# Kernel optimization log

Measured on AMD Instinct MI355X. Metric: run time of the kernel, lower is better.

## Reference

```python
import jax, jax.numpy as jnp
import numpy as np
import math

EPS = 1e-8        # numeric guard in segment intersection (matches mmcv EPSILON)
MODE_EPS = 1e-6   # module's eps
N_BOXES = 1000000


def box2corners(box):
    # box: (B, N, 5) -> corners (B, N, 4, 2)
    cx, cy, w, h, a = [box[..., i:i + 1] for i in range(5)]
    x4 = jnp.asarray([0.5, -0.5, -0.5, 0.5], box.dtype) * w   # (B,N,4)
    y4 = jnp.asarray([-0.5, -0.5, 0.5, 0.5], box.dtype) * h
    c, s = jnp.cos(a), jnp.sin(a)
    return jnp.stack([x4 * c - y4 * s + cx, x4 * s + y4 * c + cy], axis=-1)


def box_intersection(corners1, corners2):
    # all pairwise segment intersections between edges of the two boxes
    line1 = jnp.concatenate([corners1, jnp.roll(corners1, -1, axis=2)], axis=-1)  # (B,N,4,4)
    line2 = jnp.concatenate([corners2, jnp.roll(corners2, -1, axis=2)], axis=-1)
    l1 = line1[:, :, :, None, :]  # (B,N,4,1,4)
    l2 = line2[:, :, None, :, :]  # (B,N,1,4,4)
    x1, y1, x2, y2 = l1[..., 0], l1[..., 1], l1[..., 2], l1[..., 3]
    x3, y3, x4, y4 = l2[..., 0], l2[..., 1], l2[..., 2], l2[..., 3]
    num = (y4 - y3) * (x2 - x1) - (x4 - x3) * (y2 - y1)
    den_t = (x4 - x3) * (y1 - y3) - (y4 - y3) * (x1 - x3)
    t = den_t / (num + EPS)
    t_chk = jnp.where(num == 0, -1.0, t)
    mask_t = (t_chk > 0) & (t_chk < 1)
    den_u = (x2 - x1) * (y1 - y3) - (y2 - y1) * (x1 - x3)
    u = -den_u / (num + EPS)
    u_chk = jnp.where(num == 0, -1.0, u)
    mask_u = (u_chk > 0) & (u_chk < 1)
    mask = mask_t & mask_u  # (B,N,4,4)
    pts = jnp.stack([x1 + t * (x2 - x1), y1 + t * (y2 - y1)], axis=-1)
    pts = pts * mask[..., None].astype(pts.dtype)
    return pts, mask  # (B,N,4,4,2), (B,N,4,4)


def box_in_box(corners1, corners2):
    # which corners of box1 lie inside box2 (projection test)
    a = corners2[:, :, 0:1, :]
    b = corners2[:, :, 1:2, :]
    d = corners2[:, :, 3:4, :]
    ab, ad, am = b - a, d - a, corners1 - a
    p_ab = jnp.sum(ab * am, -1) / jnp.sum(ab * ab, -1)
    p_ad = jnp.sum(ad * am, -1) / jnp.sum(ad * ad, -1)
    tol = 1e-6
    return (p_ab > -tol) & (p_ab < 1 + tol) & (p_ad > -tol) & (p_ad < 1 + tol)


def intersection_area(corners1, corners2):
    # differentiable convex-intersection area via vertex sort + shoelace
    inter_pts, inter_mask = box_intersection(corners1, corners2)
    c1_in_2 = box_in_box(corners1, corners2)
    c2_in_1 = box_in_box(corners2, corners1)
    B, N = corners1.shape[:2]
    verts = jnp.concatenate([corners1, corners2, inter_pts.reshape(B, N, 16, 2)], axis=2)  # (B,N,24,2)
    mask = jnp.concatenate([c1_in_2, c2_in_1, inter_mask.reshape(B, N, 16)], axis=2)       # (B,N,24)
    num_valid = jnp.sum(mask, axis=-1, keepdims=True).astype(verts.dtype)  # (B,N,1)
    center = jnp.sum(verts * mask[..., None], axis=2) / jnp.maximum(num_valid, 1.0)  # (B,N,2)
    v = verts - center[:, :, None, :]
    ang = jnp.where(mask, jnp.arctan2(v[..., 1], v[..., 0]), 1e7)  # invalid -> end
    order = jnp.argsort(ang, axis=-1)
    v_sorted = jnp.take_along_axis(v, order[..., None], axis=2)
    m_sorted = jnp.take_along_axis(mask, order, axis=2)
    first = v_sorted[:, :, 0:1, :]
    poly = jnp.where(m_sorted[..., None], v_sorted, first)  # pad with first vertex (closes polygon)
    nxt = jnp.roll(poly, -1, axis=2)
    cross = poly[..., 0] * nxt[..., 1] - poly[..., 1] * nxt[..., 0]
    return jnp.abs(jnp.sum(cross, axis=-1)) * 0.5  # (B,N)


def diff_iou_rotated_2d(box1, box2):
    c1, c2 = box2corners(box1), box2corners(box2)
    inter = intersection_area(c1, c2)
    area1 = box1[..., 2] * box1[..., 3]
    area2 = box2[..., 2] * box2[..., 3]
    return inter / (area1 + area2 - inter)


def obb2hbb_xyxy(obb):
    cx, cy, w, h, a = obb[:, 0], obb[:, 1], obb[:, 2], obb[:, 3], obb[:, 4]
    c, s = jnp.abs(jnp.cos(a)), jnp.abs(jnp.sin(a))
    dw = (w * c + h * s) * 0.5
    dh = (w * s + h * c) * 0.5
    return jnp.stack([cx - dw, cy - dh, cx + dw, cy + dh], axis=-1)


def setup_inputs():
    key = jax.random.key(0)
    k = jax.random.split(key, 7)
    N = N_BOXES
    cxy = jax.random.uniform(k[0], (N, 2), jnp.float32, 0.0, 1024.0)
    wh = jax.random.uniform(k[1], (N, 2), jnp.float32, 8.0, 128.0)
    ang = jax.random.uniform(k[2], (N, 1), jnp.float32, -np.pi / 2, np.pi / 2)
    pred = jnp.concatenate([cxy, wh, ang], axis=-1)
    jit_xy = jax.random.uniform(k[3], (N, 2), jnp.float32, -10.0, 10.0)
    jit_wh = jax.random.uniform(k[4], (N, 2), jnp.float32, 0.8, 1.25)
    jit_a = jax.random.uniform(k[5], (N, 1), jnp.float32, -0.3, 0.3)
    target = jnp.concatenate([pred[:, :2] + jit_xy, pred[:, 2:4] * jit_wh, pred[:, 4:5] + jit_a], axis=-1)
    weight = jax.random.uniform(k[6], (N,), jnp.float32, 0.5, 1.5)
    return {"pred": pred, "target": target, "weight": weight}


def reference(pred, target, weight):
    eps = MODE_EPS
    ious = jnp.clip(diff_iou_rotated_2d(pred[None], target[None])[0], 0.0, 1.0)  # (N,)
    # enclosing HBB for penalty terms
    hp, ht = obb2hbb_xyxy(pred), obb2hbb_xyxy(target)
    en_wh = jnp.clip(jnp.maximum(hp[:, 2:], ht[:, 2:]) - jnp.minimum(hp[:, :2], ht[:, :2]), 0.0)
    c2 = en_wh[:, 0] ** 2 + en_wh[:, 1] ** 2 + eps
    rho2 = (target[:, 0] - pred[:, 0]) ** 2 + (target[:, 1] - pred[:, 1]) ** 2
    factor = 4.0 / (math.pi ** 2)
    v = factor * (jnp.arctan(target[:, 2] / (target[:, 3] + eps)) - jnp.arctan(pred[:, 2] / (pred[:, 3] + eps))) ** 2
    alpha = jax.lax.stop_gradient((ious > 0.5).astype(v.dtype) * v / (1.0 - ious + v + eps))
    cious = ious - (jnp.clip(rho2 / c2, 0.0, 1.0) + alpha * v)
    loss = (1.0 - cious) * weight
    return jnp.mean(loss)  # loss_weight=1.0, reduction='mean'
```

## Files before the change

kernel.cpp:

```cpp
#include <hip/hip_runtime.h>
#include <math.h>


#define BLOCK 256
#define NV 16
#define LDS_STRIDE 17

typedef float v2f __attribute__((ext_vector_type(2)));

struct CEList {
    int n;
    unsigned char lo[128];
    unsigned char hi[128];
};

constexpr CEList make_ces16() {
    CEList L{};
    L.n = 0;
    for (int p = 1; p < NV; p <<= 1)
        for (int k = p; k >= 1; k >>= 1)
            for (int j = k % p; j + k < NV; j += 2 * k)
                for (int i = 0; i < k; i++) {
                    int lo = i + j, hi = i + j + k;
                    if (hi < NV && (lo / (2 * p)) == (hi / (2 * p))) {
                        L.lo[L.n] = (unsigned char)lo;
                        L.hi[L.n] = (unsigned char)hi;
                        L.n++;
                    }
                }
    return L;
}

constexpr CEList CES = make_ces16();

__device__ __forceinline__ float frcp(float x) {
    return __builtin_amdgcn_rcpf(x);
}

__device__ __forceinline__ v2f splat2(float x) {
    v2f r; r.x = x; r.y = x; return r;
}

__device__ __forceinline__ float hadd2(v2f v) { return v.x + v.y; }

__device__ __forceinline__ float angle_key(float x, float y) {
    float ax = fabsf(x), ay = fabsf(y);
    float den = ax + ay;
    float r = x * frcp(den);
    r = (den > 0.f) ? r : 0.f;
    return (y >= 0.f) ? (1.f - r) : (3.f + r);
}

__device__ __forceinline__ unsigned int pack_bf2(float x, float y) {
    unsigned int bx = __float_as_uint(x) + 0x8000u;
    unsigned int by = __float_as_uint(y) + 0x8000u;
    return (by & 0xFFFF0000u) | (bx >> 16);
}

__device__ __forceinline__ float atan01(float z) {
    float z2 = z * z;
    float p = -0.01172120f;
    p = p * z2 + 0.05265332f;
    p = p * z2 - 0.11643287f;
    p = p * z2 + 0.19354346f;
    p = p * z2 - 0.33262347f;
    p = p * z2 + 0.99997726f;
    return z * p;
}

__device__ __forceinline__ float pair_loss(const float* __restrict__ p,
                                           const float* __restrict__ t,
                                           float wv,
                                           unsigned int* __restrict__ myb)
{
    const float EPSf  = 1e-8f;
    const float TOLf  = 1e-6f;
    const float MEPS  = 1e-6f;
    const float PIf   = 3.14159265358979323846f;

    float pcx = p[0], pcy = p[1], pw = p[2], ph = p[3], pa = p[4];
    float tcx = t[0], tcy = t[1], tw = t[2], th = t[3], ta = t[4];

    float ca = __cosf(pa), sa = __sinf(pa);
    float cb = __cosf(ta), sb = __sinf(ta);
    v2f C1[4], C2[4];
    {
        const float xs[4] = { 0.5f, -0.5f, -0.5f, 0.5f };
        const float ys[4] = { -0.5f, -0.5f, 0.5f, 0.5f };
        v2f R1x = { ca, sa },  R1y = { -sa, cb };
        R1y.x = -sa; R1y.y = ca;
        v2f R2x = { cb, sb },  R2y = { -sb, cb };
        R2y.x = -sb; R2y.y = cb;
        v2f CT1 = { pcx, pcy }, CT2 = { tcx, tcy };
        #pragma unroll
        for (int k = 0; k < 4; k++) {
            float x4 = xs[k] * pw, y4 = ys[k] * ph;
            C1[k] = splat2(x4) * R1x + splat2(y4) * R1y + CT1;
            float x4b = xs[k] * tw, y4b = ys[k] * th;
            C2[k] = splat2(x4b) * R2x + splat2(y4b) * R2y + CT2;
        }
    }

    v2f  V[NV];
    bool msk[NV];

    {
        v2f A  = C2[0];
        v2f AB = C2[1] - A, AD = C2[3] - A;
        float rab = frcp(hadd2(AB * AB));
        float rad = frcp(hadd2(AD * AD));
        #pragma unroll
        for (int k = 0; k < 4; k++) {
            v2f AM = C1[k] - A;
            float pab = hadd2(AB * AM) * rab;
            float pad = hadd2(AD * AM) * rad;
            msk[k] = (pab > -TOLf) && (pab < 1.f + TOLf) &&
                     (pad > -TOLf) && (pad < 1.f + TOLf);
            V[k] = C1[k];
        }
    }
    {
        v2f A  = C1[0];
        v2f AB = C1[1] - A, AD = C1[3] - A;
        float rab = frcp(hadd2(AB * AB));
        float rad = frcp(hadd2(AD * AD));
        #pragma unroll
        for (int k = 0; k < 4; k++) {
            v2f AM = C2[k] - A;
            float pab = hadd2(AB * AM) * rab;
            float pad = hadd2(AD * AM) * rad;
            msk[4 + k] = (pab > -TOLf) && (pab < 1.f + TOLf) &&
                         (pad > -TOLf) && (pad < 1.f + TOLf);
            V[4 + k] = C2[k];
        }
    }
    #pragma unroll
    for (int e1 = 0; e1 < 4; e1++) {
        v2f P1 = C1[e1];
        v2f E  = C1[(e1 + 1) & 3] - P1;
        v2f  Q[4];
        bool qm[4];
        #pragma unroll
        for (int e2 = 0; e2 < 4; e2++) {
            v2f P3 = C2[e2];
            v2f F  = C2[(e2 + 1) & 3] - P3;
            float num  = F.y * E.x - F.x * E.y;
            float rnum = frcp(num + EPSf);
            v2f D = P1 - P3;
            float den_t = F.x * D.y - F.y * D.x;
            float den_u = E.x * D.y - E.y * D.x;
            float tt = den_t * rnum;
            float uu = -den_u * rnum;
            qm[e2] = (num != 0.f) && (tt > 0.f) && (tt < 1.f)
                                  && (uu > 0.f) && (uu < 1.f);
            Q[e2] = splat2(tt) * E + P1;
        }
        bool mfL = qm[0] || qm[1];
        v2f  fL  = qm[0] ? Q[0] : Q[1];
        bool msL = qm[0] && qm[1];
        bool mfR = qm[2] || qm[3];
        v2f  fR  = qm[2] ? Q[2] : Q[3];
        bool msR = qm[2] && qm[3];
        int s0 = 8 + 2 * e1, s1 = s0 + 1;
        V[s0]   = mfL ? fL : fR;
        msk[s0] = mfL || mfR;
        v2f  t2 = msL ? Q[1] : fR;
        V[s1]   = mfL ? t2 : Q[3];
        msk[s1] = msL || (mfL && mfR) || msR;
    }

    v2f s2 = { 0.f, 0.f };
    float cnt = 0.f;
    const v2f Z2 = { 0.f, 0.f };
    #pragma unroll
    for (int k = 0; k < NV; k++) {
        s2  += msk[k] ? V[k] : Z2;
        cnt += msk[k] ? 1.f : 0.f;
    }
    float rden = frcp(fmaxf(cnt, 1.f));
    v2f cen = s2 * splat2(rden);

    unsigned int ku[NV];
    #pragma unroll
    for (int k = 0; k < NV; k++) {
        v2f R = V[k] - cen;
        myb[k] = pack_bf2(R.x, R.y);
        float a = msk[k] ? angle_key(R.x, R.y) : 1e7f;
        ku[k] = (__float_as_uint(a) & 0xFFFFFFF0u) | (unsigned int)k;
    }

    #pragma unroll
    for (int c = 0; c < CES.n; c++) {
        const int lo = CES.lo[c], hi = CES.hi[c];
        unsigned int a = ku[lo], b = ku[hi];
        ku[lo] = a < b ? a : b;
        ku[hi] = a < b ? b : a;
    }

    const unsigned int VALID_LIM = 0x49742400u;
    float gx[NV], gy[NV];
    bool  gv[NV];
    #pragma unroll
    for (int k = 0; k < NV; k++) {
        unsigned int pk = myb[ku[k] & 15u];
        gx[k] = __uint_as_float(pk << 16);
        gy[k] = __uint_as_float(pk & 0xFFFF0000u);
        gv[k] = ku[k] < VALID_LIM;
    }
    float fx = gx[0], fy = gy[0];
    float cross = 0.f;
    #pragma unroll
    for (int k = 0; k < NV; k++) {
        int kn = (k + 1) % NV;
        float axv = gv[k]  ? gx[k]  : fx, ayv = gv[k]  ? gy[k]  : fy;
        float bxv = gv[kn] ? gx[kn] : fx, byv = gv[kn] ? gy[kn] : fy;
        cross += axv * byv - ayv * bxv;
    }
    float inter = fabsf(cross) * 0.5f;

    float area1 = pw * ph, area2 = tw * th;
    float iou = inter * frcp(area1 + area2 - inter);
    iou = fminf(fmaxf(iou, 0.f), 1.f);

    float cA = fabsf(ca), sA = fabsf(sa);
    float cB = fabsf(cb), sB = fabsf(sb);
    float dw1 = (pw * cA + ph * sA) * 0.5f, dh1 = (pw * sA + ph * cA) * 0.5f;
    float dw2 = (tw * cB + th * sB) * 0.5f, dh2 = (tw * sB + th * cB) * 0.5f;
    float hp0 = pcx - dw1, hp1 = pcy - dh1, hp2 = pcx + dw1, hp3 = pcy + dh1;
    float ht0 = tcx - dw2, ht1 = tcy - dh2, ht2 = tcx + dw2, ht3 = tcy + dh2;

    float enw = fmaxf(fmaxf(hp2, ht2) - fminf(hp0, ht0), 0.f);
    float enh = fmaxf(fmaxf(hp3, ht3) - fminf(hp1, ht1), 0.f);
    float c2v = enw * enw + enh * enh + MEPS;
    float rho2 = (tcx - pcx) * (tcx - pcx) + (tcy - pcy) * (tcy - pcy);

    float factor = 4.f / (PIf * PIf);
    float r1 = tw * frcp(th + MEPS);
    float r2 = pw * frcp(ph + MEPS);
    float xd = (r1 - r2) * frcp(1.f + r1 * r2);
    float axd = fabsf(xd);
    bool  big = axd > 1.f;
    float z   = big ? frcp(axd) : axd;
    float at  = atan01(z);
    float dv  = big ? ((0.5f * PIf) - at) : at;
    float v_ = factor * dv * dv;
    float alpha = (iou > 0.5f) ? v_ * frcp(1.f - iou + v_ + MEPS) : 0.f;

    float rhoterm = fminf(fmaxf(rho2 * frcp(c2v), 0.f), 1.f);
    float ciou = iou - (rhoterm + alpha * v_);
    return (1.f - ciou) * wv;
}

__global__ __launch_bounds__(BLOCK)
void obb_ciou_kernel(const float* __restrict__ pred,
                     const float* __restrict__ tgt,
                     const float* __restrict__ wgt,
                     float* __restrict__ out,
                     int N, float invN)
{
    __shared__ unsigned int slab[BLOCK * LDS_STRIDE];
    unsigned int* myb = slab + (int)threadIdx.x * LDS_STRIDE;

    int i = blockIdx.x * BLOCK + (int)threadIdx.x;
    float loss = 0.f;
    if (i < N)
        loss = pair_loss(pred + (size_t)i * 5, tgt + (size_t)i * 5,
                         wgt[i], myb);

    #pragma unroll
    for (int off = 32; off > 0; off >>= 1)
        loss += __shfl_down(loss, off, 64);

    __shared__ float red[BLOCK / 64];
    int wave = threadIdx.x >> 6;
    int lane = threadIdx.x & 63;
    if (lane == 0) red[wave] = loss;
    __syncthreads();
    if (threadIdx.x == 0) {
        float s = 0.f;
        #pragma unroll
        for (int w = 0; w < BLOCK / 64; w++) s += red[w];
        atomicAdd(out, s * invN);
    }
}

extern "C" void kernel_launch(void* const* d_in, const int* in_sizes, int n_in,
                              void* d_out, int out_size, void* d_ws, size_t ws_size,
                              hipStream_t stream) {
    const float* pred = (const float*)d_in[0];
    const float* tgt  = (const float*)d_in[1];
    const float* wgt  = (const float*)d_in[2];
    float* out = (float*)d_out;
    int N = in_sizes[2];

    hipMemsetAsync(out, 0, sizeof(float) * (size_t)out_size, stream);

    int grid = (N + BLOCK - 1) / BLOCK;
    obb_ciou_kernel<<<grid, BLOCK, 0, stream>>>(pred, tgt, wgt, out, N,
                                                1.f / (float)N);
}
```

Measured before the change: 133.1 us.

## Compute box intersection in pred-box local frame to simplify geometry

Transforms the target box into the predicted box's local coordinate frame, so the predicted box becomes axis-aligned. Corner-in-box tests turn into absolute-value comparisons, and edge intersections reduce to one-dimensional solves against constant lines with precomputed reciprocals. This cuts the per-pair ALU and reciprocal work of the general segment-intersection code. The tolerance semantics change slightly (scaled half-extent bounds instead of projection tolerances, and no epsilon guard on the denominator), which could alter masks for degenerate or edge-touching cases.

```diff
diff --git a/kernel.cpp b/kernel.cpp
--- a/kernel.cpp
+++ b/kernel.cpp
@@ -37,12 +37,6 @@
     return __builtin_amdgcn_rcpf(x);
 }
 
-__device__ __forceinline__ v2f splat2(float x) {
-    v2f r; r.x = x; r.y = x; return r;
-}
-
-__device__ __forceinline__ float hadd2(v2f v) { return v.x + v.y; }
-
 __device__ __forceinline__ float angle_key(float x, float y) {
     float ax = fabsf(x), ay = fabsf(y);
     float den = ax + ay;
@@ -73,100 +67,108 @@
                                            float wv,
                                            unsigned int* __restrict__ myb)
 {
-    const float EPSf  = 1e-8f;
-    const float TOLf  = 1e-6f;
-    const float MEPS  = 1e-6f;
-    const float PIf   = 3.14159265358979323846f;
+    const float MEPS = 1e-6f;
+    const float PIf  = 3.14159265358979323846f;
+    const float TOLm = 1.f + 2e-6f;
 
     float pcx = p[0], pcy = p[1], pw = p[2], ph = p[3], pa = p[4];
     float tcx = t[0], tcy = t[1], tw = t[2], th = t[3], ta = t[4];
 
     float ca = __cosf(pa), sa = __sinf(pa);
     float cb = __cosf(ta), sb = __sinf(ta);
-    v2f C1[4], C2[4];
-    {
-        const float xs[4] = { 0.5f, -0.5f, -0.5f, 0.5f };
-        const float ys[4] = { -0.5f, -0.5f, 0.5f, 0.5f };
-        v2f R1x = { ca, sa },  R1y = { -sa, cb };
-        R1y.x = -sa; R1y.y = ca;
-        v2f R2x = { cb, sb },  R2y = { -sb, cb };
-        R2y.x = -sb; R2y.y = cb;
-        v2f CT1 = { pcx, pcy }, CT2 = { tcx, tcy };
-        #pragma unroll
-        for (int k = 0; k < 4; k++) {
-            float x4 = xs[k] * pw, y4 = ys[k] * ph;
-            C1[k] = splat2(x4) * R1x + splat2(y4) * R1y + CT1;
-            float x4b = xs[k] * tw, y4b = ys[k] * th;
-            C2[k] = splat2(x4b) * R2x + splat2(y4b) * R2y + CT2;
-        }
-    }
+
+    float hw1 = 0.5f * pw, hh1 = 0.5f * ph;
+    float hw2 = 0.5f * tw, hh2 = 0.5f * th;
+
+    float ddx = tcx - pcx, ddy = tcy - pcy;
+    float c2x = ddx * ca + ddy * sa;
+    float c2y = ddy * ca - ddx * sa;
+    float cd  = cb * ca + sb * sa;
+    float sd  = sb * ca - cb * sa;
+
+    float Axv = hw2 * cd,  Ayv = hw2 * sd;
+    float Bxv = -hh2 * sd, Byv = hh2 * cd;
+    float qpAx = c2x + Axv, qpAy = c2y + Ayv;
+    float qmAx = c2x - Axv, qmAy = c2y - Ayv;
+    float C0x = qpAx - Bxv, C0y = qpAy - Byv;
+    float C1x = qmAx - Bxv, C1y = qmAy - Byv;
+    float C2x = qmAx + Bxv, C2y = qmAy + Byv;
+    float C3x = qpAx + Bxv, C3y = qpAy + Byv;
 
     v2f  V[NV];
     bool msk[NV];
 
     {
-        v2f A  = C2[0];
-        v2f AB = C2[1] - A, AD = C2[3] - A;
-        float rab = frcp(hadd2(AB * AB));
-        float rad = frcp(hadd2(AD * AD));
+        float exl = -hw1 - c2x, exh = hw1 - c2x;
+        float eyl = -hh1 - c2y, eyh = hh1 - c2y;
+        float lw2 = hw2 * TOLm, lh2 = hh2 * TOLm;
+        float du, dv;
+        du = exh * cd + eyl * sd; dv = eyl * cd - exh * sd;
+        msk[0] = (fabsf(du) < lw2) && (fabsf(dv) < lh2);
+        V[0] = (v2f){ hw1, -hh1 };
+        du = exl * cd + eyl * sd; dv = eyl * cd - exl * sd;
+        msk[1] = (fabsf(du) < lw2) && (fabsf(dv) < lh2);
+        V[1] = (v2f){ -hw1, -hh1 };
+        du = exl * cd + eyh * sd; dv = eyh * cd - exl * sd;
+        msk[2] = (fabsf(du) < lw2) && (fabsf(dv) < lh2);
+        V[2] = (v2f){ -hw1, hh1 };
+        du = exh * cd + eyh * sd; dv = eyh * cd - exh * sd;
+        msk[3] = (fabsf(du) < lw2) && (fabsf(dv) < lh2);
+        V[3] = (v2f){ hw1, hh1 };
+    }
+
+    {
+        float lw1 = hw1 * TOLm, lh1 = hh1 * TOLm;
+        msk[4] = (fabsf(C0x) < lw1) && (fabsf(C0y) < lh1); V[4] = (v2f){C0x, C0y};
+        msk[5] = (fabsf(C1x) < lw1) && (fabsf(C1y) < lh1); V[5] = (v2f){C1x, C1y};
+        msk[6] = (fabsf(C2x) < lw1) && (fabsf(C2y) < lh1); V[6] = (v2f){C2x, C2y};
+        msk[7] = (fabsf(C3x) < lw1) && (fabsf(C3y) < lh1); V[7] = (v2f){C3x, C3y};
+    }
+
+    {
+        float twcd = Axv + Axv, twsd = Ayv + Ayv;
+        float thsd = -(Bxv + Bxv), thcd = Byv + Byv;
+        float rax = frcp(twcd), ray = frcp(twsd);
+        float rbx = frcp(thsd), rby = frcp(thcd);
+
+        float Sx[4]  = { C0x, C1x, C2x, C3x };
+        float Sy[4]  = { C0y, C1y, C2y, C3y };
+        float Dxe[4] = { -twcd, -thsd, twcd, thsd };
+        float Dye[4] = { -twsd, thcd, twsd, -thcd };
+        float iDx[4] = { -rax, -rbx, rax, rbx };
+        float iDy[4] = { -ray, rby, ray, -rby };
+
         #pragma unroll
-        for (int k = 0; k < 4; k++) {
-            v2f AM = C1[k] - A;
-            float pab = hadd2(AB * AM) * rab;
-            float pad = hadd2(AD * AM) * rad;
-            msk[k] = (pab > -TOLf) && (pab < 1.f + TOLf) &&
-                     (pad > -TOLf) && (pad < 1.f + TOLf);
-            V[k] = C1[k];
+        for (int e1 = 0; e1 < 4; e1++) {
+            const bool horiz = (e1 == 0) || (e1 == 2);
+            const float cc   = (e1 == 0) ? -hh1 : (e1 == 1) ? -hw1
+                             : (e1 == 2) ?  hh1 :  hw1;
+            const float lim  = horiz ? hw1 : hh1;
+            float q[4]; bool qm[4];
+            #pragma unroll
+            for (int j = 0; j < 4; j++) {
+                float u = horiz ? (cc - Sy[j]) * iDy[j]
+                                : (cc - Sx[j]) * iDx[j];
+                float w = horiz ? fmaf(u, Dxe[j], Sx[j])
+                                : fmaf(u, Dye[j], Sy[j]);
+                qm[j] = (u > -1.f) && (u < 0.f) && (fabsf(w) < lim);
+                q[j] = w;
+            }
+            bool mfL = qm[0] || qm[1];
+            float fL = qm[0] ? q[0] : q[1];
+            bool msL = qm[0] && qm[1];
+            bool mfR = qm[2] || qm[3];
+            float fR = qm[2] ? q[2] : q[3];
+            bool msR = qm[2] && qm[3];
+            int s0 = 8 + 2 * e1, s1 = s0 + 1;
+            float w0 = mfL ? fL : fR;
+            msk[s0]  = mfL || mfR;
+            float t2v = msL ? q[1] : fR;
+            float w1 = mfL ? t2v : q[3];
+            msk[s1]  = msL || (mfL && mfR) || msR;
+            V[s0] = horiz ? (v2f){ w0, cc } : (v2f){ cc, w0 };
+            V[s1] = horiz ? (v2f){ w1, cc } : (v2f){ cc, w1 };
         }
-    }
-    {
-        v2f A  = C1[0];
-        v2f AB = C1[1] - A, AD = C1[3] - A;
-        float rab = frcp(hadd2(AB * AB));
-        float rad = frcp(hadd2(AD * AD));
-        #pragma unroll
-        for (int k = 0; k < 4; k++) {
-            v2f AM = C2[k] - A;
-            float pab = hadd2(AB * AM) * rab;
-            float pad = hadd2(AD * AM) * rad;
-            msk[4 + k] = (pab > -TOLf) && (pab < 1.f + TOLf) &&
-                         (pad > -TOLf) && (pad < 1.f + TOLf);
-            V[4 + k] = C2[k];
-        }
-    }
-    #pragma unroll
-    for (int e1 = 0; e1 < 4; e1++) {
-        v2f P1 = C1[e1];
-        v2f E  = C1[(e1 + 1) & 3] - P1;
-        v2f  Q[4];
-        bool qm[4];
-        #pragma unroll
-        for (int e2 = 0; e2 < 4; e2++) {
-            v2f P3 = C2[e2];
-            v2f F  = C2[(e2 + 1) & 3] - P3;
-            float num  = F.y * E.x - F.x * E.y;
-            float rnum = frcp(num + EPSf);
-            v2f D = P1 - P3;
-            float den_t = F.x * D.y - F.y * D.x;
-            float den_u = E.x * D.y - E.y * D.x;
-            float tt = den_t * rnum;
-            float uu = -den_u * rnum;
-            qm[e2] = (num != 0.f) && (tt > 0.f) && (tt < 1.f)
-                                  && (uu > 0.f) && (uu < 1.f);
-            Q[e2] = splat2(tt) * E + P1;
-        }
-        bool mfL = qm[0] || qm[1];
-        v2f  fL  = qm[0] ? Q[0] : Q[1];
-        bool msL = qm[0] && qm[1];
-        bool mfR = qm[2] || qm[3];
-        v2f  fR  = qm[2] ? Q[2] : Q[3];
-        bool msR = qm[2] && qm[3];
-        int s0 = 8 + 2 * e1, s1 = s0 + 1;
-        V[s0]   = mfL ? fL : fR;
-        msk[s0] = mfL || mfR;
-        v2f  t2 = msL ? Q[1] : fR;
-        V[s1]   = mfL ? t2 : Q[3];
-        msk[s1] = msL || (mfL && mfR) || msR;
     }
 
     v2f s2 = { 0.f, 0.f };
@@ -178,7 +180,7 @@
         cnt += msk[k] ? 1.f : 0.f;
     }
     float rden = frcp(fmaxf(cnt, 1.f));
-    v2f cen = s2 * splat2(rden);
+    v2f cen = s2 * (v2f){ rden, rden };
 
     unsigned int ku[NV];
     #pragma unroll
```

After: 129.8 us. -2.5%, faster.
